# Optimization experiments

Hardware: AMD Instinct MI355X
Metric: run time of the kernel (lower is better)

Reference implementation:

```python
import jax, jax.numpy as jnp
import numpy as np


def setup_inputs() -> dict:
    key = jax.random.key(0)
    k1, k2, k3, k4, k5 = jax.random.split(key, 5)
    B, C, H, W = 8, 32, 64, 64
    inp = jax.random.normal(k1, (B, C, H, W), dtype=jnp.float32)
    # expected positions lie inside the image grid
    exPx = jax.random.uniform(k2, (B, H, W), dtype=jnp.float32) * (W - 1)
    exPy = jax.random.uniform(k3, (B, H, W), dtype=jnp.float32) * (H - 1)
    # positive Gaussian widths in roughly [1, 3]
    sigmax = jax.random.uniform(k4, (B, H, W), dtype=jnp.float32) * 2.0 + 1.0
    sigmay = jax.random.uniform(k5, (B, H, W), dtype=jnp.float32) * 2.0 + 1.0
    return {"input": inp, "exPx": exPx, "exPy": exPy,
            "sigmax": sigmax, "sigmay": sigmay}


def reference(input, exPx, exPy, sigmax, sigmay):
    """Gaussian-weighted spatial swap/warp (soft gather).

    For each output pixel (i, j):
      out[b,c,i,j] = sum_{u,v} G(u; exPy[b,i,j], sigmay[b,i,j])
                              * G(v; exPx[b,i,j], sigmax[b,i,j])
                              * input[b,c,u,v]  /  Z[b,i,j]
    where G is an unnormalized Gaussian and Z is the total weight mass.
    The 2D Gaussian weight is separable, so we contract rows then cols.
    """
    B, C, H, W = input.shape
    u = jnp.arange(H, dtype=input.dtype)  # source row coords (y)
    v = jnp.arange(W, dtype=input.dtype)  # source col coords (x)
    # wy: [B,H,W,H] weight over source rows u for each output pixel (i,j)
    wy = jnp.exp(-0.5 * ((u[None, None, None, :] - exPy[..., None]) / sigmay[..., None]) ** 2)
    # wx: [B,H,W,W] weight over source cols v
    wx = jnp.exp(-0.5 * ((v[None, None, None, :] - exPx[..., None]) / sigmax[..., None]) ** 2)
    # normalization mass per output pixel
    Z = wy.sum(-1) * wx.sum(-1) + jnp.asarray(1e-8, input.dtype)  # [B,H,W]
    # contract over source rows u -> [B,C,H,W,W]
    t = jnp.einsum('biju,bcuv->bcijv', wy, input)
    # contract over source cols v -> [B,C,H,W]
    out = jnp.einsum('bcijv,bijv->bcij', t, wx)
    return out / Z[:, None]
```

## Files before the change

kernel.cpp:

```cpp
#include <hip/hip_runtime.h>


#define BB 8
#define CC 32
#define HH 64
#define WW 64

typedef __attribute__((ext_vector_type(8))) short short8;
typedef __attribute__((ext_vector_type(4))) float f32x4;
typedef unsigned int uint;

__device__ __forceinline__ uint rn_bf16(float f) {
    uint u = __float_as_uint(f);
    return (u + 0x7FFFu + ((u >> 16) & 1u)) >> 16;
}

__global__ void preconvert_kernel(const float* __restrict__ x, uint* __restrict__ hi)
{
    const int n = BB * CC * HH * WW / 2;
    int idx = blockIdx.x * blockDim.x + threadIdx.x;
    for (; idx < n; idx += gridDim.x * blockDim.x) {
        const float2 d = ((const float2*)x)[idx];
        hi[idx] = rn_bf16(d.x) | (rn_bf16(d.y) << 16);
    }
}

#define WYT_OFF   0
#define WXH_OFF   17408
#define SUM_OFF   26624
#define INVZ_OFF  28672
#define LDS_BYTES 28928

__global__ __launch_bounds__(256, 4)
void swap_mfma_kernel(const uint* __restrict__ xhi,
                      const float* __restrict__ exPx, const float* __restrict__ exPy,
                      const float* __restrict__ sigmax, const float* __restrict__ sigmay,
                      float* __restrict__ out)
{
    __shared__ __align__(16) char lds[LDS_BYTES];
    const int t    = threadIdx.x;
    const int lane = t & 63;
    const int w    = t >> 6;
    const int q    = (t >> 4) & 3;
    const int ln   = t & 15;
    const int bid   = blockIdx.x;
    const int b     = bid & 7;
    const int r     = bid >> 3;
    const int chalf = r & 1;
    const int i     = r >> 1;
    const int bi    = b * 64 + i;

    float* WYT = (float*)(lds + WYT_OFF);

    {
        const int p = lane;
        const int g = w;
        const int pixBase = bi * 64 + p;
        const float ey = exPy[pixBase], ex = exPx[pixBase];
        const float isy = 1.0f / sigmay[pixBase], isx = 1.0f / sigmax[pixBase];
        float sy = 0.0f, sx = 0.0f;
        #pragma unroll
        for (int jb = 0; jb < 4; ++jb) {
            float4 wv;
            #pragma unroll
            for (int rr = 0; rr < 4; ++rr) {
                const int u = g * 16 + jb * 4 + rr;
                const float dy = ((float)u - ey) * isy;
                const float wy = __expf(-0.5f * dy * dy);
                ((float*)&wv)[rr] = wy;
                sy += wy;
            }
            *(float4*)&WYT[p * 68 + g * 16 + jb * 4] = wv;
        }
        uint* WXH = (uint*)(lds + WXH_OFF);
        #pragma unroll
        for (int j = 0; j < 8; ++j) {
            const int v0 = g * 16 + 2 * j;
            const float dx0 = ((float)v0       - ex) * isx;
            const float dx1 = ((float)(v0 + 1) - ex) * isx;
            const float wx0 = __expf(-0.5f * dx0 * dx0);
            const float wx1 = __expf(-0.5f * dx1 * dx1);
            sx += wx0 + wx1;
            WXH[p * 36 + g * 8 + j] = rn_bf16(wx0) | (rn_bf16(wx1) << 16);
        }
        float* SUMY = (float*)(lds + SUM_OFF);
        float* SUMX = SUMY + 256;
        SUMY[g * 64 + p] = sy;
        SUMX[g * 64 + p] = sx;
    }
    __syncthreads();
    float* INVZ = (float*)(lds + INVZ_OFF);
    if (t < 64) {
        float* SUMY = (float*)(lds + SUM_OFF);
        float* SUMX = SUMY + 256;
        const float sy = SUMY[t] + SUMY[64 + t] + SUMY[128 + t] + SUMY[192 + t];
        const float sx = SUMX[t] + SUMX[64 + t] + SUMX[128 + t] + SUMX[192 + t];
        INVZ[t] = 1.0f / (sy * sx + 1e-8f);
    }
    __syncthreads();

    short8 bh[4][2];
    #pragma unroll
    for (int nt = 0; nt < 4; ++nt)
        #pragma unroll
        for (int ks = 0; ks < 2; ++ks)
            bh[nt][ks] = *(const short8*)(lds + WXH_OFF + (nt * 16 + ln) * 144 + ks * 64 + q * 16);
    float invz[4];
    #pragma unroll
    for (int nt = 0; nt < 4; ++nt) invz[nt] = INVZ[nt * 16 + ln];

    const int cplane0 = b * CC + chalf * 16 + w * 4;
    const uint* xbase = xhi + (size_t)cplane0 * 2048 + ln * 32 + q * 4;
    float* obase = out + (size_t)cplane0 * 4096 + i * 64 + ln;

    for (int c = 0; c < 4; ++c) {
        const uint* xc = xbase + c * 2048;
        union { uint4 v; short8 s; } A[4][2];
        #pragma unroll
        for (int mt = 0; mt < 4; ++mt) {
            A[mt][0].v = *(const uint4*)(xc + mt * 512);
            A[mt][1].v = *(const uint4*)(xc + mt * 512 + 16);
        }
        #pragma unroll
        for (int nt = 0; nt < 4; ++nt) {
            float ps = 0.0f;
            #pragma unroll
            for (int mt = 0; mt < 4; ++mt) {
                f32x4 acc = (f32x4){0.f, 0.f, 0.f, 0.f};
                acc = __builtin_amdgcn_mfma_f32_16x16x32_bf16(A[mt][0].s, bh[nt][0], acc, 0, 0, 0);
                acc = __builtin_amdgcn_mfma_f32_16x16x32_bf16(A[mt][1].s, bh[nt][1], acc, 0, 0, 0);
                const f32x4 wv = *(const f32x4*)&WYT[(nt * 16 + ln) * 68 + mt * 16 + q * 4];
                ps += acc[0] * wv[0] + acc[1] * wv[1] + acc[2] * wv[2] + acc[3] * wv[3];
            }
            ps += __shfl_xor(ps, 16, 64);
            ps += __shfl_xor(ps, 32, 64);
            if (q == 0)
                obase[(size_t)c * 4096 + nt * 16] = ps * invz[nt];
        }
    }
}

__device__ __forceinline__ void split_pair(float f0, float f1, uint& hi, uint& lo) {
    const uint u0 = __float_as_uint(f0), u1 = __float_as_uint(f1);
    hi = (u0 >> 16) | (u1 & 0xFFFF0000u);
    const float l0 = f0 - __uint_as_float(u0 & 0xFFFF0000u);
    const float l1 = f1 - __uint_as_float(u1 & 0xFFFF0000u);
    lo = (__float_as_uint(l0) >> 16) | (__float_as_uint(l1) & 0xFFFF0000u);
}

#define FB_WYS_OFF   0
#define FB_WXH_OFF   16640
#define FB_SUM_OFF   25856
#define FB_INVZ_OFF  27904
#define FB_LDS_BYTES 28160
#define FB_RED_OFF   0

__global__ __launch_bounds__(256, 4)
void swap_fused_kernel(const float* __restrict__ inp,
                       const float* __restrict__ exPx, const float* __restrict__ exPy,
                       const float* __restrict__ sigmax, const float* __restrict__ sigmay,
                       float* __restrict__ out)
{
    __shared__ __align__(16) char lds[FB_LDS_BYTES];
    const int t = threadIdx.x;
    const int lane = t & 63, w = t >> 6, q = (t >> 4) & 3, ln = t & 15;
    const int bid = blockIdx.x;
    const int b = bid & 7, r = bid >> 3;
    const int chalf = r & 1, i = r >> 1;
    const int bi = b * 64 + i;

    float* WYS = (float*)(lds + FB_WYS_OFF);
    {
        const int p = lane, g = w;
        const int pixBase = bi * 64 + p;
        const float ey = exPy[pixBase], ex = exPx[pixBase];
        const float isy = 1.0f / sigmay[pixBase], isx = 1.0f / sigmax[pixBase];
        float sy = 0.0f, sx = 0.0f;
        #pragma unroll
        for (int k = 0; k < 16; ++k) {
            const int u = g * 16 + k;
            const float dy = ((float)u - ey) * isy;
            const float wy = __expf(-0.5f * dy * dy);
            WYS[u * 65 + p] = wy; sy += wy;
        }
        uint* WXH = (uint*)(lds + FB_WXH_OFF);
        #pragma unroll
        for (int j = 0; j < 8; ++j) {
            const int v0 = g * 16 + 2 * j;
            const float dx0 = ((float)v0 - ex) * isx;
            const float dx1 = ((float)(v0 + 1) - ex) * isx;
            const float wx0 = __expf(-0.5f * dx0 * dx0);
            const float wx1 = __expf(-0.5f * dx1 * dx1);
            sx += wx0 + wx1;
            WXH[p * 36 + g * 8 + j] = rn_bf16(wx0) | (rn_bf16(wx1) << 16);
        }
        float* SUMY = (float*)(lds + FB_SUM_OFF);
        float* SUMX = SUMY + 256;
        SUMY[g * 64 + p] = sy; SUMX[g * 64 + p] = sx;
    }
    __syncthreads();
    float* INVZ = (float*)(lds + FB_INVZ_OFF);
    if (t < 64) {
        float* SUMY = (float*)(lds + FB_SUM_OFF);
        float* SUMX = SUMY + 256;
        const float sy = SUMY[t] + SUMY[64 + t] + SUMY[128 + t] + SUMY[192 + t];
        const float sx = SUMX[t] + SUMX[64 + t] + SUMX[128 + t] + SUMX[192 + t];
        INVZ[t] = 1.0f / (sy * sx + 1e-8f);
    }
    __syncthreads();
    short8 bh[4][2];
    #pragma unroll
    for (int nt = 0; nt < 4; ++nt)
        #pragma unroll
        for (int ks = 0; ks < 2; ++ks)
            bh[nt][ks] = *(const short8*)(lds + FB_WXH_OFF + (nt * 16 + ln) * 144 + ks * 64 + q * 16);
    float wyz[4][4];
    #pragma unroll
    for (int nt = 0; nt < 4; ++nt) {
        const float iz = INVZ[nt * 16 + ln];
        #pragma unroll
        for (int rr = 0; rr < 4; ++rr)
            wyz[nt][rr] = WYS[(w * 16 + q * 4 + rr) * 65 + nt * 16 + ln] * iz;
    }
    __syncthreads();
    const int cbase = b * CC + chalf * 16;
    float* RED = (float*)(lds + FB_RED_OFF);
    const float* xrow = inp + (size_t)cbase * 4096 + (w * 16 + ln) * 64 + q * 8;
    #pragma unroll 2
    for (int c = 0; c < 16; ++c) {
        const float4* src = (const float4*)(xrow + (size_t)c * 4096);
        const float4 x0 = src[0], x1 = src[1], x2 = src[8], x3 = src[9];
        union { uint u[4]; short8 s; } Ah0, Al0, Ah1, Al1;
        split_pair(x0.x, x0.y, Ah0.u[0], Al0.u[0]);
        split_pair(x0.z, x0.w, Ah0.u[1], Al0.u[1]);
        split_pair(x1.x, x1.y, Ah0.u[2], Al0.u[2]);
        split_pair(x1.z, x1.w, Ah0.u[3], Al0.u[3]);
        split_pair(x2.x, x2.y, Ah1.u[0], Al1.u[0]);
        split_pair(x2.z, x2.w, Ah1.u[1], Al1.u[1]);
        split_pair(x3.x, x3.y, Ah1.u[2], Al1.u[2]);
        split_pair(x3.z, x3.w, Ah1.u[3], Al1.u[3]);
        f32x4 acc[4];
        #pragma unroll
        for (int nt = 0; nt < 4; ++nt) acc[nt] = (f32x4){0.f, 0.f, 0.f, 0.f};
        #pragma unroll
        for (int nt = 0; nt < 4; ++nt) {
            acc[nt] = __builtin_amdgcn_mfma_f32_16x16x32_bf16(Ah0.s, bh[nt][0], acc[nt], 0, 0, 0);
            acc[nt] = __builtin_amdgcn_mfma_f32_16x16x32_bf16(Al0.s, bh[nt][0], acc[nt], 0, 0, 0);
            acc[nt] = __builtin_amdgcn_mfma_f32_16x16x32_bf16(Ah1.s, bh[nt][1], acc[nt], 0, 0, 0);
            acc[nt] = __builtin_amdgcn_mfma_f32_16x16x32_bf16(Al1.s, bh[nt][1], acc[nt], 0, 0, 0);
        }
        #pragma unroll
        for (int nt = 0; nt < 4; ++nt) {
            float ps = acc[nt][0] * wyz[nt][0] + acc[nt][1] * wyz[nt][1]
                     + acc[nt][2] * wyz[nt][2] + acc[nt][3] * wyz[nt][3];
            ps += __shfl_xor(ps, 16, 64);
            ps += __shfl_xor(ps, 32, 64);
            if (q == 0) RED[c * 256 + w * 64 + nt * 16 + ln] = ps;
        }
    }
    __syncthreads();
    {
        const int kk = t >> 6, p = t & 63;
        #pragma unroll
        for (int g = 0; g < 4; ++g) {
            const int c = g * 4 + kk;
            const float* Rk = RED + c * 256;
            const float o = Rk[p] + Rk[64 + p] + Rk[128 + p] + Rk[192 + p];
            out[(size_t)(cbase + c) * (HH * WW) + i * 64 + p] = o;
        }
    }
}

extern "C" void kernel_launch(void* const* d_in, const int* in_sizes, int n_in,
                              void* d_out, int out_size, void* d_ws, size_t ws_size,
                              hipStream_t stream) {
    const float* inp    = (const float*)d_in[0];
    const float* exPx   = (const float*)d_in[1];
    const float* exPy   = (const float*)d_in[2];
    const float* sigmax = (const float*)d_in[3];
    const float* sigmay = (const float*)d_in[4];
    float* out = (float*)d_out;

    const size_t plane_bytes = (size_t)BB * CC * HH * WW * 2;
    if (ws_size >= plane_bytes) {
        uint* xhi = (uint*)d_ws;
        hipLaunchKernelGGL(preconvert_kernel, dim3(1024), dim3(256), 0, stream, inp, xhi);
        hipLaunchKernelGGL(swap_mfma_kernel, dim3(BB * HH * 2), dim3(256), 0, stream,
                           xhi, exPx, exPy, sigmax, sigmay, out);
    } else {
        hipLaunchKernelGGL(swap_fused_kernel, dim3(BB * HH * 2), dim3(256), 0, stream,
                           inp, exPx, exPy, sigmax, sigmay, out);
    }
}
```

Before: 97.01 us.

## Halve grid, keep Y weights in registers, double-buffer input loads across channels

Each block now handles all 32 channels of one output row, with each wave taking 8 channels, so the grid is halved and the per-block Gaussian weight setup is amortised over twice the work. The Y weights, pre-scaled by 1/Z, are held in registers instead of being re-read from LDS on every channel. Bf16 input fragments for the next channel are prefetched into a double buffer, and all four output column tiles are reduced and stored with one coalesced store per channel. The cost is much higher register pressure (launch bounds lowered to 2 blocks per SM) and fewer blocks in flight, 512 in total.

```diff
diff --git a/kernel.cpp b/kernel.cpp
--- a/kernel.cpp
+++ b/kernel.cpp
@@ -25,13 +25,13 @@
     }
 }
 
-#define WYT_OFF   0
-#define WXH_OFF   17408
-#define SUM_OFF   26624
-#define INVZ_OFF  28672
-#define LDS_BYTES 28928
-
-__global__ __launch_bounds__(256, 4)
+#define WYS_OFF   0
+#define WXH_OFF   16896
+#define SUM_OFF   26112
+#define INVZ_OFF  28160
+#define LDS_BYTES 28416
+
+__global__ __launch_bounds__(256, 2)
 void swap_mfma_kernel(const uint* __restrict__ xhi,
                       const float* __restrict__ exPx, const float* __restrict__ exPy,
                       const float* __restrict__ sigmax, const float* __restrict__ sigmay,
@@ -43,14 +43,12 @@
     const int w    = t >> 6;
     const int q    = (t >> 4) & 3;
     const int ln   = t & 15;
-    const int bid   = blockIdx.x;
-    const int b     = bid & 7;
-    const int r     = bid >> 3;
-    const int chalf = r & 1;
-    const int i     = r >> 1;
-    const int bi    = b * 64 + i;
-
-    float* WYT = (float*)(lds + WYT_OFF);
+    const int bid  = blockIdx.x;
+    const int b    = bid & 7;
+    const int i    = bid >> 3;
+    const int bi   = b * 64 + i;
+
+    float* WYS = (float*)(lds + WYS_OFF);
 
     {
         const int p = lane;
@@ -60,17 +58,12 @@
         const float isy = 1.0f / sigmay[pixBase], isx = 1.0f / sigmax[pixBase];
         float sy = 0.0f, sx = 0.0f;
         #pragma unroll
-        for (int jb = 0; jb < 4; ++jb) {
-            float4 wv;
-            #pragma unroll
-            for (int rr = 0; rr < 4; ++rr) {
-                const int u = g * 16 + jb * 4 + rr;
-                const float dy = ((float)u - ey) * isy;
-                const float wy = __expf(-0.5f * dy * dy);
-                ((float*)&wv)[rr] = wy;
-                sy += wy;
-            }
-            *(float4*)&WYT[p * 68 + g * 16 + jb * 4] = wv;
+        for (int k = 0; k < 16; ++k) {
+            const int u = g * 16 + k;
+            const float dy = ((float)u - ey) * isy;
+            const float wy = __expf(-0.5f * dy * dy);
+            WYS[u * 66 + p] = wy;
+            sy += wy;
         }
         uint* WXH = (uint*)(lds + WXH_OFF);
         #pragma unroll
@@ -105,38 +98,62 @@
         #pragma unroll
         for (int ks = 0; ks < 2; ++ks)
             bh[nt][ks] = *(const short8*)(lds + WXH_OFF + (nt * 16 + ln) * 144 + ks * 64 + q * 16);
-    float invz[4];
-    #pragma unroll
-    for (int nt = 0; nt < 4; ++nt) invz[nt] = INVZ[nt * 16 + ln];
-
-    const int cplane0 = b * CC + chalf * 16 + w * 4;
+    float wyz[4][4][4];
+    #pragma unroll
+    for (int nt = 0; nt < 4; ++nt) {
+        const float iz = INVZ[nt * 16 + ln];
+        #pragma unroll
+        for (int mt = 0; mt < 4; ++mt)
+            #pragma unroll
+            for (int rr = 0; rr < 4; ++rr)
+                wyz[mt][nt][rr] = WYS[(mt * 16 + q * 4 + rr) * 66 + nt * 16 + ln] * iz;
+    }
+
+    const int cplane0 = b * CC + w * 8;
     const uint* xbase = xhi + (size_t)cplane0 * 2048 + ln * 32 + q * 4;
-    float* obase = out + (size_t)cplane0 * 4096 + i * 64 + ln;
-
-    for (int c = 0; c < 4; ++c) {
-        const uint* xc = xbase + c * 2048;
-        union { uint4 v; short8 s; } A[4][2];
+    float* obase = out + (size_t)cplane0 * 4096 + i * 64 + lane;
+
+    union AU { uint4 v; short8 s; };
+    AU abuf[2][4][2];
+    #pragma unroll
+    for (int mt = 0; mt < 4; ++mt) {
+        abuf[0][mt][0].v = *(const uint4*)(xbase + mt * 512);
+        abuf[0][mt][1].v = *(const uint4*)(xbase + mt * 512 + 16);
+    }
+
+    #pragma unroll
+    for (int c = 0; c < 8; ++c) {
+        if (c < 7) {
+            const uint* xn = xbase + (c + 1) * 2048;
+            #pragma unroll
+            for (int mt = 0; mt < 4; ++mt) {
+                abuf[(c + 1) & 1][mt][0].v = *(const uint4*)(xn + mt * 512);
+                abuf[(c + 1) & 1][mt][1].v = *(const uint4*)(xn + mt * 512 + 16);
+            }
+        }
+        float ps[4] = {0.f, 0.f, 0.f, 0.f};
         #pragma unroll
         for (int mt = 0; mt < 4; ++mt) {
-            A[mt][0].v = *(const uint4*)(xc + mt * 512);
-            A[mt][1].v = *(const uint4*)(xc + mt * 512 + 16);
+            f32x4 acc[4];
+            #pragma unroll
+            for (int nt = 0; nt < 4; ++nt) acc[nt] = (f32x4){0.f, 0.f, 0.f, 0.f};
+            #pragma unroll
+            for (int nt = 0; nt < 4; ++nt) {
+                acc[nt] = __builtin_amdgcn_mfma_f32_16x16x32_bf16(abuf[c & 1][mt][0].s, bh[nt][0], acc[nt], 0, 0, 0);
+                acc[nt] = __builtin_amdgcn_mfma_f32_16x16x32_bf16(abuf[c & 1][mt][1].s, bh[nt][1], acc[nt], 0, 0, 0);
+            }
+            #pragma unroll
+            for (int nt = 0; nt < 4; ++nt)
+                ps[nt] += acc[nt][0] * wyz[mt][nt][0] + acc[nt][1] * wyz[mt][nt][1]
+                        + acc[nt][2] * wyz[mt][nt][2] + acc[nt][3] * wyz[mt][nt][3];
         }
         #pragma unroll
         for (int nt = 0; nt < 4; ++nt) {
-            float ps = 0.0f;
-            #pragma unroll
-            for (int mt = 0; mt < 4; ++mt) {
-                f32x4 acc = (f32x4){0.f, 0.f, 0.f, 0.f};
-                acc = __builtin_amdgcn_mfma_f32_16x16x32_bf16(A[mt][0].s, bh[nt][0], acc, 0, 0, 0);
-                acc = __builtin_amdgcn_mfma_f32_16x16x32_bf16(A[mt][1].s, bh[nt][1], acc, 0, 0, 0);
-                const f32x4 wv = *(const f32x4*)&WYT[(nt * 16 + ln) * 68 + mt * 16 + q * 4];
-                ps += acc[0] * wv[0] + acc[1] * wv[1] + acc[2] * wv[2] + acc[3] * wv[3];
-            }
-            ps += __shfl_xor(ps, 16, 64);
-            ps += __shfl_xor(ps, 32, 64);
-            if (q == 0)
-                obase[(size_t)c * 4096 + nt * 16] = ps * invz[nt];
-        }
+            ps[nt] += __shfl_xor(ps[nt], 16, 64);
+            ps[nt] += __shfl_xor(ps[nt], 32, 64);
+        }
+        const float po = (q == 0) ? ps[0] : (q == 1) ? ps[1] : (q == 2) ? ps[2] : ps[3];
+        obase[(size_t)c * 4096] = po;
     }
 }
 
@@ -285,7 +302,7 @@
     if (ws_size >= plane_bytes) {
         uint* xhi = (uint*)d_ws;
         hipLaunchKernelGGL(preconvert_kernel, dim3(1024), dim3(256), 0, stream, inp, xhi);
-        hipLaunchKernelGGL(swap_mfma_kernel, dim3(BB * HH * 2), dim3(256), 0, stream,
+        hipLaunchKernelGGL(swap_mfma_kernel, dim3(BB * HH), dim3(256), 0, stream,
                            xhi, exPx, exPy, sigmax, sigmay, out);
     } else {
         hipLaunchKernelGGL(swap_fused_kernel, dim3(BB * HH * 2), dim3(256), 0, stream,
```

New measurement: 80.74 us. 1.2x faster.
